# Performance work log

Hardware: AMD Instinct MI355X
Metric: run time of the kernel (lower is better)

## Reference

```python
import jax, jax.numpy as jnp
import numpy as np
from jax import lax

KERNEL = 512

def squash(x, axis=-1):
    sn = jnp.sum(x * x, axis=axis, keepdims=True)
    scale = sn / (1.0 + sn)
    return scale * x / jnp.sqrt(sn + 1e-8)

def setup_inputs() -> dict:
    key = jax.random.key(0)
    ks = jax.random.split(key, 6)
    x = jax.random.normal(ks[0], (4096, 1, 1008), dtype=jnp.float32)
    a = jax.random.uniform(ks[1], (128, 1, 1), dtype=jnp.float32) * 5.0 + 0.1
    w = jax.random.uniform(ks[2], (128, 1, 1), dtype=jnp.float32) * 150.0 + 1.0
    conv_w = jax.random.normal(ks[3], (256, 128, 16), dtype=jnp.float32) * 0.02
    conv_b = jnp.zeros((256,), dtype=jnp.float32)
    W_caps = jax.random.normal(ks[4], (288, 4, 16, 8), dtype=jnp.float32) * 0.01
    return {"x": x, "a": a, "w": w, "conv_w": conv_w, "conv_b": conv_b, "W_caps": W_caps}

def reference(x, a, w, conv_w, conv_b, W_caps):
    # --- WavConv1d: generate wavelet weights on the fly ---
    t = jnp.linspace(-1.0, 1.0, KERNEL, dtype=jnp.float32).reshape(1, 1, KERNEL)
    a_safe = jnp.clip(a, 1e-5, None)
    t_scaled = t / a_safe
    wav_w = jnp.cos(w * t) * jnp.exp(-0.5 * t_scaled ** 2)  # [128,1,512]
    h = lax.conv_general_dilated(x, wav_w, window_strides=(16,), padding='VALID',
                                 dimension_numbers=('NCH', 'OIH', 'NCH'))  # [B,128,32]
    # --- PrimaryCaps1d ---
    p = lax.conv_general_dilated(h, conv_w, window_strides=(2,), padding='VALID',
                                 dimension_numbers=('NCH', 'OIH', 'NCH'))  # [B,256,9]
    p = p + conv_b[None, :, None]
    B = p.shape[0]
    u = squash(p.reshape(B, -1, 8))  # [B,288,8]
    # --- ClassCaps with dynamic routing ---
    # u_hat[b,c,d,o] = sum_i W_caps[c,d,o,i] * u[b,c,i]
    u_hat = jnp.einsum('cdoi,bci->bcdo', W_caps, u)  # [B,288,4,16]
    b_ij = jnp.zeros((B, u_hat.shape[1], u_hat.shape[2], 1), dtype=u_hat.dtype)
    num_routing = 3
    for i in range(num_routing):
        c_ij = jax.nn.softmax(b_ij, axis=2)                      # [B,288,4,1]
        s_j = jnp.sum(c_ij * u_hat, axis=1, keepdims=True)       # [B,1,4,16]
        v_j = squash(s_j, axis=-1)                               # [B,1,4,16]
        if i < num_routing - 1:
            agreement = jnp.sum(u_hat * v_j, axis=-1, keepdims=True)
            b_ij = b_ij + agreement
    v = jnp.squeeze(v_j, axis=1)          # [B,4,16]
    probs = jnp.linalg.norm(v, axis=-1)   # [B,4]
    return probs, jnp.squeeze(c_ij, axis=-1)  # [B,4], [B,288,4]
```

## Files before the change

kernel.cpp:

```cpp
#include <hip/hip_runtime.h>
#include <hip/hip_bf16.h>
#include <math.h>

typedef __attribute__((ext_vector_type(4))) short short4v;
typedef __attribute__((ext_vector_type(8))) short short8;
typedef __attribute__((ext_vector_type(4))) float f32x4;
typedef __attribute__((ext_vector_type(2))) float f32x2;
typedef _Float16 half8 __attribute__((ext_vector_type(8)));

#define BATCH   4096
#define XLEN    1008
#define NOC1    128
#define NPOS    32
#define NOC2    256
#define NQ      9
#define NCAPS   288
#define NDIM    8

#define BWH_OFF   0
#define BPH_OFF   131072
#define H2_OFF    1179648
#define U_OFF     34734080

static __device__ __forceinline__ short f2h(float v) {
    _Float16 h = (_Float16)v;
    return *reinterpret_cast<short*>(&h);
}

static __device__ __forceinline__ f32x2 pkfma(float a, f32x2 b, f32x2 c) {
    f32x2 av = {a, a};
    return av * b + c;
}

template <int CTRL>
static __device__ __forceinline__ float dpp_addf(float x) {
    int y = __builtin_amdgcn_update_dpp(0, __builtin_bit_cast(int, x),
                                        CTRL, 0xf, 0xf, true);
    return x + __builtin_bit_cast(float, y);
}
static __device__ __forceinline__ float rowsum16(float x) {
    x = dpp_addf<0xB1>(x);
    x = dpp_addf<0x4E>(x);
    x = dpp_addf<0x141>(x);
    x = dpp_addf<0x140>(x);
    return x;
}

__global__ __launch_bounds__(256) void k_pack(const float* __restrict__ a,
                                              const float* __restrict__ w,
                                              const float* __restrict__ cw,
                                              short* __restrict__ bwh,
                                              short* __restrict__ bph) {
    int bid = blockIdx.x;
    int tid = threadIdx.x;
    if (bid < 256) {
        int idx = bid * 256 + tid;
        int e    = idx & 7;
        int lane = (idx >> 3) & 63;
        int s    = (idx >> 9) & 15;
        int nt   = idx >> 13;
        int oc = nt * 16 + (lane & 15);
        int k  = s * 32 + (lane >> 4) * 8 + e;
        float t  = -1.0f + 2.0f * (float)k / 511.0f;
        float av = fmaxf(a[oc], 1e-5f);
        float ts = t / av;
        bwh[idx] = f2h(cosf(w[oc] * t) * expf(-0.5f * ts * ts));
    } else {
        int o = (bid - 256) * 256 + tid;
        int e    = o & 7;
        int lane = (o >> 3) & 63;
        int s    = (o >> 9) & 63;
        int nt   = o >> 15;
        int n  = nt * 16 + (lane & 15);
        int j  = lane >> 4;
        int kk = s >> 2;
        int ic = (s & 3) * 32 + j * 8 + e;
        bph[o] = f2h(cw[(n * NOC1 + ic) * 16 + kk]);
    }
}

__global__ __launch_bounds__(512, 4) void k_wavconv_mfma(
        const float* __restrict__ x,
        const short* __restrict__ bwh,
        short* __restrict__ h2) {
    __shared__ short xl[8][1512];

    int tid = threadIdx.x;
    int b0  = blockIdx.x * 8;

    for (int i4 = tid; i4 < 2016; i4 += 512) {
        int b  = i4 / 252;
        int e4 = i4 - b * 252;
        float4 v = *(const float4*)(x + (size_t)(b0 + b) * XLEN + e4 * 4);
        int i    = e4 * 4;
        int slot = i + 8 * (i >> 4);
        short4v hv;
        hv.x = f2h(v.x); hv.y = f2h(v.y); hv.z = f2h(v.z); hv.w = f2h(v.w);
        *(short4v*)&xl[b][slot] = hv;
    }
    __syncthreads();

    int lane = tid & 63;
    int w    = tid >> 6;
    int col  = lane & 15;
    int rg   = lane >> 4;

    f32x4 acc[2][8];
    f32x4 z = {0.f, 0.f, 0.f, 0.f};
#pragma unroll
    for (int tl = 0; tl < 2; ++tl)
#pragma unroll
        for (int nt = 0; nt < 8; ++nt) acc[tl][nt] = z;

    for (int s = 0; s < 16; ++s) {
        half8 Bh[8];
#pragma unroll
        for (int nt = 0; nt < 8; ++nt) {
            size_t off = ((size_t)(nt * 16 + s) * 64 + lane) * 8;
            Bh[nt] = __builtin_bit_cast(half8, *(const short8*)(bwh + off));
        }
#pragma unroll
        for (int tl = 0; tl < 2; ++tl) {
            int pos  = tl * 16 + col;
            int i    = (pos + 2 * s) * 16 + rg * 8;
            int slot = i + 8 * (i >> 4);
            half8 ah = __builtin_bit_cast(half8, *(const short8*)&xl[w][slot]);
#pragma unroll
            for (int nt = 0; nt < 8; ++nt)
                acc[tl][nt] = __builtin_amdgcn_mfma_f32_16x16x32_f16(ah, Bh[nt], acc[tl][nt], 0, 0, 0);
        }
    }

    int b = b0 + w;
#pragma unroll
    for (int tl = 0; tl < 2; ++tl) {
        int ph = tl * 16;
#pragma unroll
        for (int nt = 0; nt < 8; ++nt) {
            int oc = nt * 16 + col;
#pragma unroll
            for (int r = 0; r < 4; ++r) {
                int pos = ph + rg * 4 + r;
                h2[((size_t)b * NPOS + pos) * NOC1 + oc] = f2h(acc[tl][nt][r]);
            }
        }
    }
}

__global__ __launch_bounds__(512, 4) void k_conv_mfma(const short* __restrict__ h2,
                                                      const short* __restrict__ bph,
                                                      const float* __restrict__ cb,
                                                      float* __restrict__ u) {
    __shared__ char smem[66048];
    short* Ald   = (short*)smem;
    float* p_lds = (float*)smem;

    int tid  = threadIdx.x;
    int w    = tid >> 6;
    int lane = tid & 63;
    int col  = lane & 15;
    int rg   = lane >> 4;
    int b0   = blockIdx.x * 8;

    {
        const short8* src = (const short8*)(h2 + (size_t)b0 * NPOS * NOC1);
#pragma unroll
        for (int i = 0; i < 8; ++i) {
            int g    = tid + 512 * i;
            short8 v = src[g];
            int row  = g >> 4;
            int slot = (g & 15) ^ ((row >> 5) & 7);
            *(short8*)&Ald[row * 128 + slot * 8] = v;
        }
        if (tid < 32) {
            short8 zz = {0, 0, 0, 0, 0, 0, 0, 0};
            *(short8*)&Ald[4096 * 8 + tid * 8] = zz;
        }
    }
    __syncthreads();

    f32x4 acc[5][2];
    f32x4 z = {0.f, 0.f, 0.f, 0.f};
#pragma unroll
    for (int mt = 0; mt < 5; ++mt) { acc[mt][0] = z; acc[mt][1] = z; }

    int rowb[5];
#pragma unroll
    for (int mt = 0; mt < 5; ++mt) {
        int m = mt * 16 + col;
        rowb[mt] = (m & 7) * 32 + 2 * (m >> 3);
    }

    for (int s = 0; s < 64; ++s) {
        int kk    = s >> 2;
        int icb8  = (s & 3) * 4;
        short8 ar[5];
#pragma unroll
        for (int mt = 0; mt < 5; ++mt) {
            int row  = rowb[mt] + kk;
            int slot = (icb8 + rg) ^ ((row >> 5) & 7);
            ar[mt] = *(const short8*)&Ald[row * 128 + slot * 8];
        }
#pragma unroll
        for (int n = 0; n < 2; ++n) {
            size_t bo = ((size_t)((w + n * 8) * 64 + s) * 64 + lane) * 8;
            half8 Bh = __builtin_bit_cast(half8, *(const short8*)(bph + bo));
#pragma unroll
            for (int mt = 0; mt < 5; ++mt)
                acc[mt][n] = __builtin_amdgcn_mfma_f32_16x16x32_f16(
                    __builtin_bit_cast(half8, ar[mt]), Bh, acc[mt][n], 0, 0, 0);
        }
    }
    __syncthreads();

    int oc2l = w * 16 + col;
    for (int n = 0; n < 2; ++n) {
        float bias = cb[n * 128 + oc2l];
#pragma unroll
        for (int mt = 0; mt < 5; ++mt)
#pragma unroll
            for (int r = 0; r < 4; ++r) {
                int m = mt * 16 + rg * 4 + r;
                if (m < 72)
                    p_lds[(m & 7) * 1152 + oc2l * 9 + (m >> 3)] = acc[mt][n][r] + bias;
            }
        __syncthreads();
        for (int idx = tid; idx < 1152; idx += 512) {
            int lb = idx / 144;
            int cl = idx - lb * 144;
            float* ppt = &p_lds[lb * 1152 + cl * 8];
            float sn = 0.f;
#pragma unroll
            for (int i = 0; i < NDIM; ++i) sn = fmaf(ppt[i], ppt[i], sn);
            float sc = sn / (1.f + sn) / sqrtf(sn + 1e-8f);
            float* ug = u + ((size_t)(b0 + lb) * (NCAPS * NDIM) + (n * 144 + cl) * 8);
            float4 u0 = make_float4(ppt[0] * sc, ppt[1] * sc, ppt[2] * sc, ppt[3] * sc);
            float4 u1 = make_float4(ppt[4] * sc, ppt[5] * sc, ppt[6] * sc, ppt[7] * sc);
            ((float4*)ug)[0] = u0;
            ((float4*)ug)[1] = u1;
        }
        __syncthreads();
    }
}

__global__ __launch_bounds__(1024, 8) void k_routing(const float* __restrict__ u,
                                                     const float* __restrict__ Wc,
                                                     float* __restrict__ out) {
    __shared__ float b_lds[2][NCAPS * 4];
    __shared__ float c_lds[2][NCAPS * 4];
    __shared__ float part_lds[2][1024];
    __shared__ float v_lds[2][64];

    int tid = threadIdx.x;
    int b0  = blockIdx.x * 2;

    int g = tid >> 6;
    int l = tid & 63;
    int d = l >> 4;
    int o = l & 15;
    int gu = __builtin_amdgcn_readfirstlane(g);

    const float* ub0 = u + (size_t)(b0 + 0) * (NCAPS * NDIM) + gu * 18 * NDIM;
    const float* ub1 = u + (size_t)(b0 + 1) * (NCAPS * NDIM) + gu * 18 * NDIM;

    f32x2 uh[18];
#pragma unroll
    for (int c = 0; c < 18; ++c) {
        int cap = gu * 18 + c;
        const float4* W4 = (const float4*)(Wc + ((size_t)cap * 512) + l * 8);
        float4 A  = W4[0];
        float4 Bv = W4[1];
        f32x2 u0 = {ub0[c * 8 + 0], ub1[c * 8 + 0]};
        f32x2 u1 = {ub0[c * 8 + 1], ub1[c * 8 + 1]};
        f32x2 u2 = {ub0[c * 8 + 2], ub1[c * 8 + 2]};
        f32x2 u3 = {ub0[c * 8 + 3], ub1[c * 8 + 3]};
        f32x2 u4 = {ub0[c * 8 + 4], ub1[c * 8 + 4]};
        f32x2 u5 = {ub0[c * 8 + 5], ub1[c * 8 + 5]};
        f32x2 u6 = {ub0[c * 8 + 6], ub1[c * 8 + 6]};
        f32x2 u7 = {ub0[c * 8 + 7], ub1[c * 8 + 7]};
        f32x2 t = (f32x2){A.x, A.x} * u0;
        t = pkfma(A.y,  u1, t);
        t = pkfma(A.z,  u2, t);
        t = pkfma(A.w,  u3, t);
        t = pkfma(Bv.x, u4, t);
        t = pkfma(Bv.y, u5, t);
        t = pkfma(Bv.z, u6, t);
        t = pkfma(Bv.w, u7, t);
        uh[c] = t;
    }

    for (int r = 0; r < 3; ++r) {
        if (r > 0) {
            __builtin_amdgcn_wave_barrier();
            for (int i = l; i < 36; i += 64) {
                int bb = (i >= 18) ? 1 : 0;
                int cl = i - bb * 18;
                int c  = gu * 18 + cl;
                float4 bv = *(const float4*)&b_lds[bb][c * 4];
                float m  = fmaxf(fmaxf(bv.x, bv.y), fmaxf(bv.z, bv.w));
                float e0 = expf(bv.x - m), e1 = expf(bv.y - m);
                float e2 = expf(bv.z - m), e3 = expf(bv.w - m);
                float inv = 1.f / (e0 + e1 + e2 + e3);
                e0 *= inv; e1 *= inv; e2 *= inv; e3 *= inv;
                *(float4*)&c_lds[bb][c * 4] = make_float4(e0, e1, e2, e3);
                if (r == 2) {
                    *(float4*)(out + 16384 + ((size_t)(b0 + bb) * NCAPS + c) * 4) =
                        make_float4(e0, e1, e2, e3);
                }
            }
            __builtin_amdgcn_wave_barrier();
        }

        f32x2 p = {0.f, 0.f};
        if (r == 0) {
#pragma unroll
            for (int c = 0; c < 18; ++c)
                p = pkfma(0.25f, uh[c], p);
        } else {
#pragma unroll
            for (int c = 0; c < 18; ++c) {
                f32x2 c2 = {c_lds[0][(g * 18 + c) * 4 + d],
                            c_lds[1][(g * 18 + c) * 4 + d]};
                p = c2 * uh[c] + p;
            }
        }
        part_lds[0][tid] = p.x;
        part_lds[1][tid] = p.y;
        __syncthreads();

        if (tid < 128) {
            int bb = tid >> 6;
            int ll = tid & 63;
            float sv = 0.f;
#pragma unroll
            for (int k = 0; k < 16; ++k) sv += part_lds[bb][ll + 64 * k];
            float sq = rowsum16(sv * sv);
            float sc = sq / (1.f + sq) / sqrtf(sq + 1e-8f);
            float v  = sv * sc;
            v_lds[bb][ll] = v;
            if (r == 2) {
                float vv = rowsum16(v * v);
                if ((ll & 15) == 0)
                    out[(size_t)(b0 + bb) * 4 + (ll >> 4)] = sqrtf(vv);
            }
        }
        __syncthreads();

        if (r < 2) {
            f32x2 v01 = {v_lds[0][l], v_lds[1][l]};
#pragma unroll
            for (int c = 0; c < 18; ++c) {
                f32x2 t2 = uh[c] * v01;
                float t0 = rowsum16(t2.x);
                float t1 = rowsum16(t2.y);
                if (o == 0) {
                    if (r == 0) {
                        b_lds[0][(g * 18 + c) * 4 + d] = t0;
                        b_lds[1][(g * 18 + c) * 4 + d] = t1;
                    } else {
                        b_lds[0][(g * 18 + c) * 4 + d] += t0;
                        b_lds[1][(g * 18 + c) * 4 + d] += t1;
                    }
                }
            }
        }
    }
}

extern "C" void kernel_launch(void* const* d_in, const int* in_sizes, int n_in,
                              void* d_out, int out_size, void* d_ws, size_t ws_size,
                              hipStream_t stream) {
    const float* x      = (const float*)d_in[0];
    const float* a      = (const float*)d_in[1];
    const float* w      = (const float*)d_in[2];
    const float* conv_w = (const float*)d_in[3];
    const float* conv_b = (const float*)d_in[4];
    const float* W_caps = (const float*)d_in[5];
    float* out = (float*)d_out;
    char* ws   = (char*)d_ws;

    short*  bwh = (short*)(ws + BWH_OFF);
    short*  bph = (short*)(ws + BPH_OFF);
    short*  h2  = (short*)(ws + H2_OFF);
    float*  u   = (float*)(ws + U_OFF);

    k_pack<<<2304, 256, 0, stream>>>(a, w, conv_w, bwh, bph);
    k_wavconv_mfma<<<BATCH / 8, 512, 0, stream>>>(x, bwh, h2);
    k_conv_mfma<<<BATCH / 8, 512, 0, stream>>>(h2, bph, conv_b, u);
    k_routing<<<BATCH / 2, 1024, 0, stream>>>(u, W_caps, out);
}
```

Baseline: 278.9 us.

## Fuse wavelet conv and primary-caps conv into one kernel via LDS handoff

Merges the wavelet convolution and the primary capsule convolution into a single kernel. The fp16 intermediate h2 (about 33 MB) no longer round-trips through global memory; each block writes its MFMA results straight into the swizzled LDS layout the second stage already reads. Launch bounds drop to 2 blocks per CU, which lowers occupancy, and the whole 66 KB LDS buffer is shared and reused by both stages.

```diff
diff --git a/kernel.cpp b/kernel.cpp
--- a/kernel.cpp
+++ b/kernel.cpp
@@ -19,8 +19,7 @@
 
 #define BWH_OFF   0
 #define BPH_OFF   131072
-#define H2_OFF    1179648
-#define U_OFF     34734080
+#define U_OFF     1179648
 
 static __device__ __forceinline__ short f2h(float v) {
     _Float16 h = (_Float16)v;
@@ -79,14 +78,23 @@
     }
 }
 
-__global__ __launch_bounds__(512, 4) void k_wavconv_mfma(
+__global__ __launch_bounds__(512, 2) void k_wavcaps(
         const float* __restrict__ x,
         const short* __restrict__ bwh,
-        short* __restrict__ h2) {
-    __shared__ short xl[8][1512];
-
-    int tid = threadIdx.x;
-    int b0  = blockIdx.x * 8;
+        const short* __restrict__ bph,
+        const float* __restrict__ cb,
+        float* __restrict__ u) {
+    __shared__ char smem[66048];
+    short* Ald   = (short*)smem;
+    short* xl    = (short*)smem;
+    float* p_lds = (float*)smem;
+
+    int tid  = threadIdx.x;
+    int w    = tid >> 6;
+    int lane = tid & 63;
+    int col  = lane & 15;
+    int rg   = lane >> 4;
+    int b0   = blockIdx.x * 8;
 
     for (int i4 = tid; i4 < 2016; i4 += 512) {
         int b  = i4 / 252;
@@ -96,82 +104,50 @@
         int slot = i + 8 * (i >> 4);
         short4v hv;
         hv.x = f2h(v.x); hv.y = f2h(v.y); hv.z = f2h(v.z); hv.w = f2h(v.w);
-        *(short4v*)&xl[b][slot] = hv;
+        *(short4v*)&xl[(size_t)b * 1512 + slot] = hv;
     }
     __syncthreads();
 
-    int lane = tid & 63;
-    int w    = tid >> 6;
-    int col  = lane & 15;
-    int rg   = lane >> 4;
-
-    f32x4 acc[2][8];
-    f32x4 z = {0.f, 0.f, 0.f, 0.f};
-#pragma unroll
-    for (int tl = 0; tl < 2; ++tl)
-#pragma unroll
-        for (int nt = 0; nt < 8; ++nt) acc[tl][nt] = z;
-
-    for (int s = 0; s < 16; ++s) {
-        half8 Bh[8];
-#pragma unroll
-        for (int nt = 0; nt < 8; ++nt) {
-            size_t off = ((size_t)(nt * 16 + s) * 64 + lane) * 8;
-            Bh[nt] = __builtin_bit_cast(half8, *(const short8*)(bwh + off));
-        }
-#pragma unroll
-        for (int tl = 0; tl < 2; ++tl) {
-            int pos  = tl * 16 + col;
-            int i    = (pos + 2 * s) * 16 + rg * 8;
-            int slot = i + 8 * (i >> 4);
-            half8 ah = __builtin_bit_cast(half8, *(const short8*)&xl[w][slot]);
+    {
+        f32x4 acc[2][8];
+        f32x4 z = {0.f, 0.f, 0.f, 0.f};
+#pragma unroll
+        for (int tl = 0; tl < 2; ++tl)
+#pragma unroll
+            for (int nt = 0; nt < 8; ++nt) acc[tl][nt] = z;
+
+        for (int s = 0; s < 16; ++s) {
+            half8 Bh[8];
+#pragma unroll
+            for (int nt = 0; nt < 8; ++nt) {
+                size_t off = ((size_t)(nt * 16 + s) * 64 + lane) * 8;
+                Bh[nt] = __builtin_bit_cast(half8, *(const short8*)(bwh + off));
+            }
+#pragma unroll
+            for (int tl = 0; tl < 2; ++tl) {
+                int pos  = tl * 16 + col;
+                int i    = (pos + 2 * s) * 16 + rg * 8;
+                int slot = i + 8 * (i >> 4);
+                half8 ah = __builtin_bit_cast(half8, *(const short8*)&xl[(size_t)w * 1512 + slot]);
+#pragma unroll
+                for (int nt = 0; nt < 8; ++nt)
+                    acc[tl][nt] = __builtin_amdgcn_mfma_f32_16x16x32_f16(ah, Bh[nt], acc[tl][nt], 0, 0, 0);
+            }
+        }
+        __syncthreads();
+
+#pragma unroll
+        for (int tl = 0; tl < 2; ++tl)
 #pragma unroll
             for (int nt = 0; nt < 8; ++nt)
-                acc[tl][nt] = __builtin_amdgcn_mfma_f32_16x16x32_f16(ah, Bh[nt], acc[tl][nt], 0, 0, 0);
-        }
-    }
-
-    int b = b0 + w;
-#pragma unroll
-    for (int tl = 0; tl < 2; ++tl) {
-        int ph = tl * 16;
-#pragma unroll
-        for (int nt = 0; nt < 8; ++nt) {
-            int oc = nt * 16 + col;
-#pragma unroll
-            for (int r = 0; r < 4; ++r) {
-                int pos = ph + rg * 4 + r;
-                h2[((size_t)b * NPOS + pos) * NOC1 + oc] = f2h(acc[tl][nt][r]);
-            }
-        }
-    }
-}
-
-__global__ __launch_bounds__(512, 4) void k_conv_mfma(const short* __restrict__ h2,
-                                                      const short* __restrict__ bph,
-                                                      const float* __restrict__ cb,
-                                                      float* __restrict__ u) {
-    __shared__ char smem[66048];
-    short* Ald   = (short*)smem;
-    float* p_lds = (float*)smem;
-
-    int tid  = threadIdx.x;
-    int w    = tid >> 6;
-    int lane = tid & 63;
-    int col  = lane & 15;
-    int rg   = lane >> 4;
-    int b0   = blockIdx.x * 8;
-
-    {
-        const short8* src = (const short8*)(h2 + (size_t)b0 * NPOS * NOC1);
-#pragma unroll
-        for (int i = 0; i < 8; ++i) {
-            int g    = tid + 512 * i;
-            short8 v = src[g];
-            int row  = g >> 4;
-            int slot = (g & 15) ^ ((row >> 5) & 7);
-            *(short8*)&Ald[row * 128 + slot * 8] = v;
-        }
+#pragma unroll
+                for (int r = 0; r < 4; ++r) {
+                    int pos  = tl * 16 + rg * 4 + r;
+                    int row  = w * 32 + pos;
+                    int oc   = nt * 16 + col;
+                    int slot = (oc >> 3) ^ (w & 7);
+                    Ald[row * 128 + slot * 8 + (oc & 7)] = f2h(acc[tl][nt][r]);
+                }
         if (tid < 32) {
             short8 zz = {0, 0, 0, 0, 0, 0, 0, 0};
             *(short8*)&Ald[4096 * 8 + tid * 8] = zz;
@@ -381,11 +357,9 @@
 
     short*  bwh = (short*)(ws + BWH_OFF);
     short*  bph = (short*)(ws + BPH_OFF);
-    short*  h2  = (short*)(ws + H2_OFF);
     float*  u   = (float*)(ws + U_OFF);
 
     k_pack<<<2304, 256, 0, stream>>>(a, w, conv_w, bwh, bph);
-    k_wavconv_mfma<<<BATCH / 8, 512, 0, stream>>>(x, bwh, h2);
-    k_conv_mfma<<<BATCH / 8, 512, 0, stream>>>(h2, bph, conv_b, u);
+    k_wavcaps<<<BATCH / 8, 512, 0, stream>>>(x, bwh, bph, conv_b, u);
     k_routing<<<BATCH / 2, 1024, 0, stream>>>(u, W_caps, out);
 }
```

New measurement: 253.1 us. 9.2% less time.
